# Optimization experiments

Measured on AMD Instinct MI355X. Metric: run time of the kernel, lower is better.

The kernel has to match this reference:

```python
import jax, jax.numpy as jnp
import numpy as np
from jax import lax

K = 3      # kernel_size
PAD = 1    # padding
OG = 2     # offset groups


def _conv2d(x, w, b):
    y = lax.conv_general_dilated(x, w, (1, 1), [(PAD, PAD), (PAD, PAD)],
                                 dimension_numbers=('NCHW', 'OIHW', 'NCHW'))
    return y + b[None, :, None, None]


def _deform_conv2d(x, offset, mask, weight):
    # torchvision-style modulated deform_conv2d (v2), stride=1, dilation=1,
    # zero out-of-bounds, offset layout [B, OG*K*K*2, H, W] with (dy, dx) pairs.
    B, C, H, W = x.shape
    O = weight.shape[0]
    K2 = K * K
    Cg = C // OG

    ki, kj = jnp.meshgrid(jnp.arange(K), jnp.arange(K), indexing='ij')
    ki = ki.reshape(K2)
    kj = kj.reshape(K2)
    base_y = jnp.arange(H)[None, :] - PAD + ki[:, None]   # [K2, H]
    base_x = jnp.arange(W)[None, :] - PAD + kj[:, None]   # [K2, W]

    off = offset.reshape(B, OG, K2, 2, H, W)
    py = off[:, :, :, 0] + base_y[None, None, :, :, None].astype(x.dtype)  # [B,OG,K2,H,W]
    px = off[:, :, :, 1] + base_x[None, None, :, None, :].astype(x.dtype)
    m = mask.reshape(B, OG, K2, H, W)

    y0f = jnp.floor(py)
    x0f = jnp.floor(px)
    wy1 = py - y0f   # bilinear weights, grads flow through py/px
    wx1 = px - x0f
    y0 = y0f.astype(jnp.int32)
    x0 = x0f.astype(jnp.int32)
    y1 = y0 + 1
    x1 = x0 + 1

    img = x.reshape(B, OG, Cg, H * W)

    def gather(yi, xi):
        valid = (yi >= 0) & (yi < H) & (xi >= 0) & (xi < W)
        idx = jnp.clip(yi, 0, H - 1) * W + jnp.clip(xi, 0, W - 1)          # [B,OG,K2,H,W]
        v = jnp.take_along_axis(img[:, :, :, None, :],
                                idx.reshape(B, OG, 1, K2, H * W), axis=-1)
        return v.reshape(B, OG, Cg, K2, H, W) * valid[:, :, None].astype(x.dtype)

    v00 = gather(y0, x0)
    v01 = gather(y0, x1)
    v10 = gather(y1, x0)
    v11 = gather(y1, x1)

    wy1e = wy1[:, :, None]   # [B,OG,1,K2,H,W]
    wx1e = wx1[:, :, None]
    val = (v00 * (1 - wy1e) * (1 - wx1e)
           + v01 * (1 - wy1e) * wx1e
           + v10 * wy1e * (1 - wx1e)
           + v11 * wy1e * wx1e)
    val = val * m[:, :, None]                               # modulation mask

    wr = weight.reshape(O, OG, Cg, K2)
    return jnp.einsum('ogck,bgckhw->bohw', wr, val)


def setup_inputs() -> dict:
    key = jax.random.key(0)
    k1, k2, k3, k4, k5 = jax.random.split(key, 5)
    B, C, O, H, W = 4, 64, 64, 128, 128
    K2 = K * K
    x = jax.random.normal(k1, (B, C, H, W), dtype=jnp.float32)
    w_main = jax.random.normal(k2, (O, C, K, K), dtype=jnp.float32) / np.sqrt(C * K2)
    w_off = jax.random.normal(k3, (2 * OG * K2, C, K, K), dtype=jnp.float32) * 0.01
    b_off = jax.random.normal(k4, (2 * OG * K2,), dtype=jnp.float32) * 0.01
    w_mask = jnp.full((OG * K2, C, K, K), 0.5, dtype=jnp.float32)  # init_mask = 0.5
    b_mask = jax.random.normal(k5, (OG * K2,), dtype=jnp.float32) * 0.01
    return {"x": x, "w_main": w_main, "w_off": w_off, "b_off": b_off,
            "w_mask": w_mask, "b_mask": b_mask}


def reference(x, w_main, w_off, b_off, w_mask, b_mask):
    offset = _conv2d(x, w_off, b_off)
    mask = jax.nn.sigmoid(_conv2d(x, w_mask, b_mask))
    return _deform_conv2d(x, offset, mask, w_main)
```

## Files before the change

kernel.cpp:

```cpp
#include <hip/hip_runtime.h>
#include <math.h>

#define BB 4
#define C 64
#define O 64
#define H 128
#define W 128
#define K2 9
#define HW (H*W)
#define NOFF 36

typedef __bf16 bf16;
typedef bf16 bf16x8 __attribute__((ext_vector_type(8)));
typedef float f32x4 __attribute__((ext_vector_type(4)));
typedef unsigned short u16x8 __attribute__((ext_vector_type(8)));
typedef unsigned int u32x4 __attribute__((ext_vector_type(4)));

#define BSTR 55
#define B2STR 19
#define VSTR 36
#define SSTR 72
#define VAL_OFF 9728
#define SMEM_BYTES 23552
#define WFRAG 18432
#define NW_TOTAL 73728

__device__ inline unsigned short f2h_bits(float f) {
  _Float16 h = (_Float16)f;
  return __builtin_bit_cast(unsigned short, h);
}
__device__ inline float h2f(unsigned short u) {
  return (float)__builtin_bit_cast(_Float16, u);
}

__global__ __launch_bounds__(256) void prep_all(
    const float* __restrict__ x, const float* __restrict__ w_main,
    const float* __restrict__ w_off, const float* __restrict__ w_mask,
    unsigned short* __restrict__ xT16, bf16* __restrict__ wfC,
    bf16* __restrict__ wfM) {
  __shared__ float tile[64][68];
  int tid = threadIdx.x;
  int b = blockIdx.x >> 8;
  int p0 = (blockIdx.x & 255) * 64;
#pragma unroll
  for (int it = 0; it < 4; ++it) {
    int c = it * 16 + (tid >> 4);
    int p4 = (tid & 15) * 4;
    *(f32x4*)&tile[c][p4] =
        *(const f32x4*)(x + (size_t)(b * C + c) * HW + p0 + p4);
  }
  __syncthreads();
#pragma unroll
  for (int it = 0; it < 2; ++it) {
    int t = it * 256 + tid;
    int p = t >> 3;
    int h8 = t & 7;
    u16x8 o;
#pragma unroll
    for (int j = 0; j < 8; ++j) {
      bf16 v = (bf16)tile[h8 * 8 + j][p];
      o[j] = __builtin_bit_cast(unsigned short, v);
    }
    *(u16x8*)&xT16[(size_t)(b * HW + p0 + p) * C + h8 * 8] = o;
  }
  int i = blockIdx.x * 256 + tid;
  if (i < NW_TOTAL) {
    int which = (i >= 36864);
    int ii = which ? i - 36864 : i;
    int j = ii & 7;
    int l = (ii >> 3) & 63;
    int rest = ii >> 9;
    int to = rest & 3;
    int kk = (rest >> 2) % 9;
    int ph = (rest >> 2) / 9;
    int m = to * 16 + (l & 15);
    int u = kk * 32 + (l >> 4) * 8 + j;
    int tap = u >> 5;
    int c1 = u & 31;
    if (!which) {
      int c = ph * 32 + c1;
      float v = (m < NOFF) ? w_off[(m * C + c) * K2 + tap]
                : (m < 54) ? w_mask[((m - NOFF) * C + c) * K2 + tap]
                           : 0.f;
      wfC[ii] = (bf16)v;
    } else {
      wfM[ii] = (bf16)w_main[(m * C + ph * 32 + c1) * K2 + tap];
    }
  }
}

__global__ __launch_bounds__(256, 6) void fused_deform(
    const bf16* __restrict__ xT, const bf16* __restrict__ wfC,
    const bf16* __restrict__ wfM, const float* __restrict__ b_off,
    const float* __restrict__ b_mask, float* __restrict__ out) {
  __shared__ __align__(16) char smem[SMEM_BYTES];
  bf16* stage = (bf16*)smem;
  float* bufF = (float*)smem;
  u32x4* buf2 = (u32x4*)smem;
  float* valF = (float*)smem;
  bf16* val = (bf16*)(smem + VAL_OFF);

  const int tid = threadIdx.x;
  const int lane = tid & 63;
  const int wv = tid >> 6;
  const int n16 = lane & 15;
  const int q4 = lane >> 4;
  const int to = wv;
  const int pg = tid >> 3;
  const int ch = tid & 7;

  const int g8 = blockIdx.x & 7;
  const int slot = blockIdx.x >> 3;
  const int b = g8 >> 1;
  const int ti = (g8 & 1) * 256 + slot;
  const int h0 = ti >> 2;
  const int w0 = (ti & 3) * 32;
  const bf16* xb = xT + (size_t)b * HW * C;

  bf16x8 zero8;
#pragma unroll
  for (int j = 0; j < 8; ++j) zero8[j] = (bf16)0.f;

#pragma unroll
  for (int it = 0; it < 4; ++it) {
    int id = it * 256 + tid;
    if (id < 816) {
      int chk = id & 7;
      int rest = id >> 3;
      int wp = rest % 34;
      int r = rest / 34;
      int yy = h0 + r - 1;
      int xx = w0 + wp - 1;
      bf16x8 v = zero8;
      if ((unsigned)yy < (unsigned)H && (unsigned)xx < (unsigned)W)
        v = *(const bf16x8*)(xb + (size_t)((yy << 7) + xx) * C + chk * 8);
      *(bf16x8*)(stage + (r * 34 + wp) * SSTR + chk * 8) = v;
    }
  }
  __syncthreads();
  f32x4 accC[2] = {{0.f,0.f,0.f,0.f},{0.f,0.f,0.f,0.f}};
#pragma unroll 1
  for (int ph = 0; ph < 2; ++ph) {
#pragma unroll
    for (int kk = 0; kk < 9; ++kk) {
      bf16x8 afr = *(const bf16x8*)(wfC +
          (size_t)(((ph * 9 + kk) * 4 + to) * 64 + lane) * 8);
#pragma unroll
      for (int nt = 0; nt < 2; ++nt) {
        bf16x8 bfr = *(const bf16x8*)(stage +
            ((kk / 3) * 34 + nt * 16 + n16 + kk % 3) * SSTR + ph * 32 + q4 * 8);
        accC[nt] = __builtin_amdgcn_mfma_f32_16x16x32_bf16(afr, bfr, accC[nt], 0, 0, 0);
      }
    }
  }
  __syncthreads();

#pragma unroll
  for (int nt = 0; nt < 2; ++nt)
#pragma unroll
    for (int r = 0; r < 4; ++r) {
      int o = to * 16 + q4 * 4 + r;
      int p = nt * 16 + n16;
      float a = accC[nt][r];
      if (o < NOFF) {
        bufF[p * BSTR + o] = a + b_off[o];
      } else if (o < 54) {
        float s = a + b_mask[o - NOFF];
        bufF[p * BSTR + o] = 1.f / (1.f + __expf(-s));
      }
    }
  __syncthreads();

  unsigned int rW0[3], rW1[3], rCo[3];
#pragma unroll
  for (int it = 0; it < 3; ++it) {
    int t = it * 256 + tid;
    if (t < 576) {
      int p = t & 31;
      int gk = t >> 5;
      int g = gk / 9, tap = gk % 9;
      float offy = bufF[p * BSTR + 2 * gk];
      float offx = bufF[p * BSTR + 2 * gk + 1];
      float m = bufF[p * BSTR + NOFF + gk];
      float py = offy + (float)(h0 + tap / 3 - 1);
      float px = offx + (float)(w0 + p + tap % 3 - 1);
      float y0f = floorf(py), x0f = floorf(px);
      float wy1 = py - y0f, wx1 = px - x0f;
      float wy0 = 1.f - wy1, wx0 = 1.f - wx1;
      int y0 = (int)y0f, x0 = (int)x0f;
      int y1 = y0 + 1, x1 = x0 + 1;
      bool y0ok = (unsigned)y0 < (unsigned)H, y1ok = (unsigned)y1 < (unsigned)H;
      bool x0ok = (unsigned)x0 < (unsigned)W, x1ok = (unsigned)x1 < (unsigned)W;
      float w00 = (y0ok && x0ok) ? wy0 * wx0 * m : 0.f;
      float w01 = (y0ok && x1ok) ? wy0 * wx1 * m : 0.f;
      float w10 = (y1ok && x0ok) ? wy1 * wx0 * m : 0.f;
      float w11 = (y1ok && x1ok) ? wy1 * wx1 * m : 0.f;
      unsigned int y0c = (unsigned)min(max(y0, 0), H - 1);
      unsigned int y1c = (unsigned)min(max(y1, 0), H - 1);
      unsigned int x0c = (unsigned)min(max(x0, 0), W - 1);
      unsigned int x1c = (unsigned)min(max(x1, 0), W - 1);
      rW0[it] = (unsigned)f2h_bits(w00) | ((unsigned)f2h_bits(w01) << 16);
      rW1[it] = (unsigned)f2h_bits(w10) | ((unsigned)f2h_bits(w11) << 16);
      rCo[it] = y0c | (x0c << 8) | (y1c << 16) | (x1c << 24);
    }
  }
  __syncthreads();
#pragma unroll
  for (int it = 0; it < 3; ++it) {
    int t = it * 256 + tid;
    if (t < 576) {
      int p = t & 31;
      int gk = t >> 5;
      u32x4 pk = {rW0[it], rW1[it], rCo[it], 0u};
      buf2[p * B2STR + gk] = pk;
    }
  }
  __syncthreads();

  f32x4 accM[2] = {{0.f,0.f,0.f,0.f},{0.f,0.f,0.f,0.f}};
  const bf16* bb = xb + ch * 8;
  const int gg = ch >> 2;
#pragma unroll 1
  for (int kc = 0; kc < 3; ++kc) {
    if (kc) __syncthreads();
#pragma unroll
    for (int t = 0; t < 3; ++t) {
      int tap = kc * 3 + t;
      u32x4 t4 = buf2[pg * B2STR + gg * 9 + tap];
      float w00 = h2f(t4.x & 0xffff), w01 = h2f(t4.x >> 16);
      float w10 = h2f(t4.y & 0xffff), w11 = h2f(t4.y >> 16);
      int r0 = (int)(t4.z & 255) << 7;
      int x0 = (int)((t4.z >> 8) & 255);
      int r1 = (int)((t4.z >> 16) & 255) << 7;
      int x1 = (int)(t4.z >> 24);
      bf16x8 v00 = *(const bf16x8*)(bb + (size_t)(r0 + x0) * C);
      bf16x8 v01 = *(const bf16x8*)(bb + (size_t)(r0 + x1) * C);
      bf16x8 v10 = *(const bf16x8*)(bb + (size_t)(r1 + x0) * C);
      bf16x8 v11 = *(const bf16x8*)(bb + (size_t)(r1 + x1) * C);
      bf16x8 res;
#pragma unroll
      for (int j = 0; j < 8; ++j) {
        float v = (float)v00[j] * w00 + (float)v01[j] * w01 +
                  (float)v10[j] * w10 + (float)v11[j] * w11;
        res[j] = (bf16)v;
      }
      *(bf16x8*)(val + (t * 32 + pg) * SSTR + ch * 8) = res;
    }
    __syncthreads();
#pragma unroll
    for (int t = 0; t < 3; ++t) {
      int tap = kc * 3 + t;
#pragma unroll
      for (int g = 0; g < 2; ++g) {
        bf16x8 afr = *(const bf16x8*)(wfM + (size_t)g * WFRAG +
            (size_t)((tap * 4 + to) * 64 + lane) * 8);
#pragma unroll
        for (int nt = 0; nt < 2; ++nt) {
          bf16x8 bfr = *(const bf16x8*)(val +
              (t * 32 + nt * 16 + n16) * SSTR + g * 32 + q4 * 8);
          accM[nt] = __builtin_amdgcn_mfma_f32_16x16x32_bf16(afr, bfr, accM[nt], 0, 0, 0);
        }
      }
    }
  }

  __syncthreads();
#pragma unroll
  for (int nt = 0; nt < 2; ++nt)
#pragma unroll
    for (int r = 0; r < 4; ++r)
      valF[(to * 16 + q4 * 4 + r) * VSTR + nt * 16 + n16] = accM[nt][r];
  __syncthreads();
  {
    float* ob = out + (size_t)b * O * HW + (h0 << 7) + w0;
#pragma unroll
    for (int it = 0; it < 2; ++it) {
      int id = it * 256 + tid;
      int o = id >> 3, seg = id & 7;
      f32x4 v = *(f32x4*)&valF[o * VSTR + seg * 4];
      *(f32x4*)&ob[(size_t)o * HW + seg * 4] = v;
    }
  }
}

extern "C" void kernel_launch(void* const* d_in, const int* in_sizes, int n_in,
                              void* d_out, int out_size, void* d_ws,
                              size_t ws_size, hipStream_t stream) {
  const float* x = (const float*)d_in[0];
  const float* w_main = (const float*)d_in[1];
  const float* w_off = (const float*)d_in[2];
  const float* b_off = (const float*)d_in[3];
  const float* w_mask = (const float*)d_in[4];
  const float* b_mask = (const float*)d_in[5];
  float* out = (float*)d_out;

  unsigned short* xT16 = (unsigned short*)d_ws;
  bf16* wfC = (bf16*)(xT16 + (size_t)BB * HW * C);
  bf16* wfM = wfC + 36864;

  prep_all<<<1024, 256, 0, stream>>>(x, w_main, w_off, w_mask, xT16, wfC, wfM);
  fused_deform<<<2048, 256, 0, stream>>>((const bf16*)xT16, wfC, wfM, b_off,
                                         b_mask, out);
}
```

Baseline: 108.7 us.

## Double-buffer bilinear sample tiles to overlap gathers with MFMA

Splits the shared-memory sample buffer into two halves and software-pipelines the tap-chunk loop: the gathers for the next three taps are issued before the MFMAs on the current chunk, then blended and stored to the other buffer afterwards. This hides global gather latency behind matrix work and removes one barrier per iteration. In exchange, shared memory per block grows and the occupancy hint drops from 6 to 4 blocks per CU, and holding the prefetched vectors raises register pressure.

```diff
diff --git a/kernel.cpp b/kernel.cpp
--- a/kernel.cpp
+++ b/kernel.cpp
@@ -21,7 +21,8 @@
 #define VSTR 36
 #define SSTR 72
 #define VAL_OFF 9728
-#define SMEM_BYTES 23552
+#define VAL1_OFF 23552
+#define SMEM_BYTES 37376
 #define WFRAG 18432
 #define NW_TOTAL 73728
 
@@ -89,7 +90,7 @@
   }
 }
 
-__global__ __launch_bounds__(256, 6) void fused_deform(
+__global__ __launch_bounds__(256, 4) void fused_deform(
     const bf16* __restrict__ xT, const bf16* __restrict__ wfC,
     const bf16* __restrict__ wfM, const float* __restrict__ b_off,
     const float* __restrict__ b_mask, float* __restrict__ out) {
@@ -98,7 +99,8 @@
   float* bufF = (float*)smem;
   u32x4* buf2 = (u32x4*)smem;
   float* valF = (float*)smem;
-  bf16* val = (bf16*)(smem + VAL_OFF);
+  bf16* val0 = (bf16*)(smem + VAL_OFF);
+  bf16* val1 = (bf16*)(smem + VAL1_OFF);
 
   const int tid = threadIdx.x;
   const int lane = tid & 63;
@@ -220,33 +222,53 @@
   f32x4 accM[2] = {{0.f,0.f,0.f,0.f},{0.f,0.f,0.f,0.f}};
   const bf16* bb = xb + ch * 8;
   const int gg = ch >> 2;
+
+#pragma unroll
+  for (int t = 0; t < 3; ++t) {
+    u32x4 t4 = buf2[pg * B2STR + gg * 9 + t];
+    float w00 = h2f(t4.x & 0xffff), w01 = h2f(t4.x >> 16);
+    float w10 = h2f(t4.y & 0xffff), w11 = h2f(t4.y >> 16);
+    int r0 = (int)(t4.z & 255) << 7;
+    int x0 = (int)((t4.z >> 8) & 255);
+    int r1 = (int)((t4.z >> 16) & 255) << 7;
+    int x1 = (int)(t4.z >> 24);
+    bf16x8 v00 = *(const bf16x8*)(bb + (size_t)(r0 + x0) * C);
+    bf16x8 v01 = *(const bf16x8*)(bb + (size_t)(r0 + x1) * C);
+    bf16x8 v10 = *(const bf16x8*)(bb + (size_t)(r1 + x0) * C);
+    bf16x8 v11 = *(const bf16x8*)(bb + (size_t)(r1 + x1) * C);
+    bf16x8 res;
+#pragma unroll
+    for (int j = 0; j < 8; ++j) {
+      float v = (float)v00[j] * w00 + (float)v01[j] * w01 +
+                (float)v10[j] * w10 + (float)v11[j] * w11;
+      res[j] = (bf16)v;
+    }
+    *(bf16x8*)(val0 + (t * 32 + pg) * SSTR + ch * 8) = res;
+  }
+  __syncthreads();
+
 #pragma unroll 1
   for (int kc = 0; kc < 3; ++kc) {
-    if (kc) __syncthreads();
-#pragma unroll
-    for (int t = 0; t < 3; ++t) {
-      int tap = kc * 3 + t;
-      u32x4 t4 = buf2[pg * B2STR + gg * 9 + tap];
-      float w00 = h2f(t4.x & 0xffff), w01 = h2f(t4.x >> 16);
-      float w10 = h2f(t4.y & 0xffff), w11 = h2f(t4.y >> 16);
-      int r0 = (int)(t4.z & 255) << 7;
-      int x0 = (int)((t4.z >> 8) & 255);
-      int r1 = (int)((t4.z >> 16) & 255) << 7;
-      int x1 = (int)(t4.z >> 24);
-      bf16x8 v00 = *(const bf16x8*)(bb + (size_t)(r0 + x0) * C);
-      bf16x8 v01 = *(const bf16x8*)(bb + (size_t)(r0 + x1) * C);
-      bf16x8 v10 = *(const bf16x8*)(bb + (size_t)(r1 + x0) * C);
-      bf16x8 v11 = *(const bf16x8*)(bb + (size_t)(r1 + x1) * C);
-      bf16x8 res;
-#pragma unroll
-      for (int j = 0; j < 8; ++j) {
-        float v = (float)v00[j] * w00 + (float)v01[j] * w01 +
-                  (float)v10[j] * w10 + (float)v11[j] * w11;
-        res[j] = (bf16)v;
-      }
-      *(bf16x8*)(val + (t * 32 + pg) * SSTR + ch * 8) = res;
-    }
-    __syncthreads();
+    bf16* cur = (kc & 1) ? val1 : val0;
+    bf16* nxt = (kc & 1) ? val0 : val1;
+    bf16x8 hv[3][4];
+    unsigned hwA[3], hwB[3];
+    if (kc < 2) {
+#pragma unroll
+      for (int t = 0; t < 3; ++t) {
+        u32x4 t4 = buf2[pg * B2STR + gg * 9 + (kc + 1) * 3 + t];
+        hwA[t] = t4.x;
+        hwB[t] = t4.y;
+        int r0 = (int)(t4.z & 255) << 7;
+        int x0 = (int)((t4.z >> 8) & 255);
+        int r1 = (int)((t4.z >> 16) & 255) << 7;
+        int x1 = (int)(t4.z >> 24);
+        hv[t][0] = *(const bf16x8*)(bb + (size_t)(r0 + x0) * C);
+        hv[t][1] = *(const bf16x8*)(bb + (size_t)(r0 + x1) * C);
+        hv[t][2] = *(const bf16x8*)(bb + (size_t)(r1 + x0) * C);
+        hv[t][3] = *(const bf16x8*)(bb + (size_t)(r1 + x1) * C);
+      }
+    }
 #pragma unroll
     for (int t = 0; t < 3; ++t) {
       int tap = kc * 3 + t;
@@ -256,15 +278,30 @@
             (size_t)((tap * 4 + to) * 64 + lane) * 8);
 #pragma unroll
         for (int nt = 0; nt < 2; ++nt) {
-          bf16x8 bfr = *(const bf16x8*)(val +
+          bf16x8 bfr = *(const bf16x8*)(cur +
               (t * 32 + nt * 16 + n16) * SSTR + g * 32 + q4 * 8);
           accM[nt] = __builtin_amdgcn_mfma_f32_16x16x32_bf16(afr, bfr, accM[nt], 0, 0, 0);
         }
       }
     }
-  }
-
-  __syncthreads();
+    if (kc < 2) {
+#pragma unroll
+      for (int t = 0; t < 3; ++t) {
+        float w00 = h2f(hwA[t] & 0xffff), w01 = h2f(hwA[t] >> 16);
+        float w10 = h2f(hwB[t] & 0xffff), w11 = h2f(hwB[t] >> 16);
+        bf16x8 res;
+#pragma unroll
+        for (int j = 0; j < 8; ++j) {
+          float v = (float)hv[t][0][j] * w00 + (float)hv[t][1][j] * w01 +
+                    (float)hv[t][2][j] * w10 + (float)hv[t][3][j] * w11;
+          res[j] = (bf16)v;
+        }
+        *(bf16x8*)(nxt + (t * 32 + pg) * SSTR + ch * 8) = res;
+      }
+    }
+    __syncthreads();
+  }
+
 #pragma unroll
   for (int nt = 0; nt < 2; ++nt)
 #pragma unroll
```

New measurement: 113.6 us. 4.5% more time.

## Swizzle LDS tiles with XOR layout and split sampling buffers to shrink shared memory

Applied to the files above, without the earlier changes.

Replaces the padded-stride LDS layout for the staged input tile and the sampled value tile with an unpadded 64-element row using an XOR chunk swizzle. This avoids bank conflicts without padding. The packed per-sample weight/coordinate record is split into three separate u32 arrays written directly, which drops a register staging pass and a barrier. The value tile now aliases the stage buffer, cutting LDS use enough to raise the occupancy hint from 6 to 8 blocks. Higher occupancy may increase register pressure, and the aliasing depends on the barrier order being correct.

```diff
diff --git a/kernel.cpp b/kernel.cpp
--- a/kernel.cpp
+++ b/kernel.cpp
@@ -17,11 +17,12 @@
 typedef unsigned int u32x4 __attribute__((ext_vector_type(4)));
 
 #define BSTR 55
-#define B2STR 19
 #define VSTR 36
-#define SSTR 72
-#define VAL_OFF 9728
-#define SMEM_BYTES 23552
+#define VAL_BYTES 12288
+#define B2A_OFF 12288
+#define B2B_OFF 14592
+#define B2C_OFF 16896
+#define SMEM_BYTES 19200
 #define WFRAG 18432
 #define NW_TOTAL 73728
 
@@ -31,6 +32,9 @@
 }
 __device__ inline float h2f(unsigned short u) {
   return (float)__builtin_bit_cast(_Float16, u);
+}
+__device__ inline int soff(int row, int chunk) {
+  return row * 64 + ((chunk ^ (row & 7)) * 8);
 }
 
 __global__ __launch_bounds__(256) void prep_all(
@@ -38,7 +42,7 @@
     const float* __restrict__ w_off, const float* __restrict__ w_mask,
     unsigned short* __restrict__ xT16, bf16* __restrict__ wfC,
     bf16* __restrict__ wfM) {
-  __shared__ float tile[64][68];
+  __shared__ float tile[64][69];
   int tid = threadIdx.x;
   int b = blockIdx.x >> 8;
   int p0 = (blockIdx.x & 255) * 64;
@@ -89,16 +93,18 @@
   }
 }
 
-__global__ __launch_bounds__(256, 6) void fused_deform(
+__global__ __launch_bounds__(256, 8) void fused_deform(
     const bf16* __restrict__ xT, const bf16* __restrict__ wfC,
     const bf16* __restrict__ wfM, const float* __restrict__ b_off,
     const float* __restrict__ b_mask, float* __restrict__ out) {
   __shared__ __align__(16) char smem[SMEM_BYTES];
   bf16* stage = (bf16*)smem;
   float* bufF = (float*)smem;
-  u32x4* buf2 = (u32x4*)smem;
   float* valF = (float*)smem;
-  bf16* val = (bf16*)(smem + VAL_OFF);
+  bf16* val = (bf16*)smem;
+  unsigned int* buf2a = (unsigned int*)(smem + B2A_OFF);
+  unsigned int* buf2b = (unsigned int*)(smem + B2B_OFF);
+  unsigned int* buf2c = (unsigned int*)(smem + B2C_OFF);
 
   const int tid = threadIdx.x;
   const int lane = tid & 63;
@@ -134,7 +140,7 @@
       bf16x8 v = zero8;
       if ((unsigned)yy < (unsigned)H && (unsigned)xx < (unsigned)W)
         v = *(const bf16x8*)(xb + (size_t)((yy << 7) + xx) * C + chk * 8);
-      *(bf16x8*)(stage + (r * 34 + wp) * SSTR + chk * 8) = v;
+      *(bf16x8*)(stage + soff(r * 34 + wp, chk)) = v;
     }
   }
   __syncthreads();
@@ -147,8 +153,8 @@
           (size_t)(((ph * 9 + kk) * 4 + to) * 64 + lane) * 8);
 #pragma unroll
       for (int nt = 0; nt < 2; ++nt) {
-        bf16x8 bfr = *(const bf16x8*)(stage +
-            ((kk / 3) * 34 + nt * 16 + n16 + kk % 3) * SSTR + ph * 32 + q4 * 8);
+        int row = (kk / 3) * 34 + nt * 16 + n16 + kk % 3;
+        bf16x8 bfr = *(const bf16x8*)(stage + soff(row, ph * 4 + q4));
         accC[nt] = __builtin_amdgcn_mfma_f32_16x16x32_bf16(afr, bfr, accC[nt], 0, 0, 0);
       }
     }
@@ -171,14 +177,13 @@
     }
   __syncthreads();
 
-  unsigned int rW0[3], rW1[3], rCo[3];
 #pragma unroll
   for (int it = 0; it < 3; ++it) {
     int t = it * 256 + tid;
     if (t < 576) {
       int p = t & 31;
       int gk = t >> 5;
-      int g = gk / 9, tap = gk % 9;
+      int tap = gk % 9;
       float offy = bufF[p * BSTR + 2 * gk];
       float offx = bufF[p * BSTR + 2 * gk + 1];
       float m = bufF[p * BSTR + NOFF + gk];
@@ -199,20 +204,10 @@
       unsigned int y1c = (unsigned)min(max(y1, 0), H - 1);
       unsigned int x0c = (unsigned)min(max(x0, 0), W - 1);
       unsigned int x1c = (unsigned)min(max(x1, 0), W - 1);
-      rW0[it] = (unsigned)f2h_bits(w00) | ((unsigned)f2h_bits(w01) << 16);
-      rW1[it] = (unsigned)f2h_bits(w10) | ((unsigned)f2h_bits(w11) << 16);
-      rCo[it] = y0c | (x0c << 8) | (y1c << 16) | (x1c << 24);
-    }
-  }
-  __syncthreads();
-#pragma unroll
-  for (int it = 0; it < 3; ++it) {
-    int t = it * 256 + tid;
-    if (t < 576) {
-      int p = t & 31;
-      int gk = t >> 5;
-      u32x4 pk = {rW0[it], rW1[it], rCo[it], 0u};
-      buf2[p * B2STR + gk] = pk;
+      int idx = p * 18 + gk;
+      buf2a[idx] = (unsigned)f2h_bits(w00) | ((unsigned)f2h_bits(w01) << 16);
+      buf2b[idx] = (unsigned)f2h_bits(w10) | ((unsigned)f2h_bits(w11) << 16);
+      buf2c[idx] = y0c | (x0c << 8) | (y1c << 16) | (x1c << 24);
     }
   }
   __syncthreads();
@@ -226,13 +221,16 @@
 #pragma unroll
     for (int t = 0; t < 3; ++t) {
       int tap = kc * 3 + t;
-      u32x4 t4 = buf2[pg * B2STR + gg * 9 + tap];
-      float w00 = h2f(t4.x & 0xffff), w01 = h2f(t4.x >> 16);
-      float w10 = h2f(t4.y & 0xffff), w11 = h2f(t4.y >> 16);
-      int r0 = (int)(t4.z & 255) << 7;
-      int x0 = (int)((t4.z >> 8) & 255);
-      int r1 = (int)((t4.z >> 16) & 255) << 7;
-      int x1 = (int)(t4.z >> 24);
+      int idx = pg * 18 + gg * 9 + tap;
+      unsigned wA = buf2a[idx];
+      unsigned wB = buf2b[idx];
+      unsigned co = buf2c[idx];
+      float w00 = h2f(wA & 0xffff), w01 = h2f(wA >> 16);
+      float w10 = h2f(wB & 0xffff), w11 = h2f(wB >> 16);
+      int r0 = (int)(co & 255) << 7;
+      int x0 = (int)((co >> 8) & 255);
+      int r1 = (int)((co >> 16) & 255) << 7;
+      int x1 = (int)(co >> 24);
       bf16x8 v00 = *(const bf16x8*)(bb + (size_t)(r0 + x0) * C);
       bf16x8 v01 = *(const bf16x8*)(bb + (size_t)(r0 + x1) * C);
       bf16x8 v10 = *(const bf16x8*)(bb + (size_t)(r1 + x0) * C);
@@ -244,7 +242,7 @@
                   (float)v10[j] * w10 + (float)v11[j] * w11;
         res[j] = (bf16)v;
       }
-      *(bf16x8*)(val + (t * 32 + pg) * SSTR + ch * 8) = res;
+      *(bf16x8*)(val + soff(t * 32 + pg, ch)) = res;
     }
     __syncthreads();
 #pragma unroll
@@ -256,8 +254,8 @@
             (size_t)((tap * 4 + to) * 64 + lane) * 8);
 #pragma unroll
         for (int nt = 0; nt < 2; ++nt) {
-          bf16x8 bfr = *(const bf16x8*)(val +
-              (t * 32 + nt * 16 + n16) * SSTR + g * 32 + q4 * 8);
+          int row = t * 32 + nt * 16 + n16;
+          bf16x8 bfr = *(const bf16x8*)(val + soff(row, g * 4 + q4));
           accM[nt] = __builtin_amdgcn_mfma_f32_16x16x32_bf16(afr, bfr, accM[nt], 0, 0, 0);
         }
       }
```

Measured after the change: 105.2 us. 1.03x faster.
